# Kernel optimization log

Hardware: AMD Instinct MI355X
Metric: run time of the kernel (lower is better)

The kernel has to match this reference:

```python
import jax, jax.numpy as jnp
import numpy as np

B, STREAM, IN_CH = 128, 512, 4
EXTRA, GROUPS, DEPTH = 5, 2, 3
STEP, LENGTH = 16, 32
RNN, OUT = 256, 10
C = IN_CH + 1 + EXTRA              # augmented channels: original + time + 1x1-conv
SIG_C = C + C * C + C ** 3          # signature channels per group at depth 3
W = (STREAM - LENGTH) // STEP + 1   # number of sliding windows = GRU steps
F = GROUPS * SIG_C                  # GRU input features


def _outer(a, b):
    # flattened tensor (outer) product on last axis: (...,m),(...,n)->(...,m*n)
    return (a[..., :, None] * b[..., None, :]).reshape(a.shape[:-1] + (a.shape[-1] * b.shape[-1],))


def _chen_step(S, dx):
    # Chen's identity: S <- S (tensor) exp(dx). S is a tuple of flattened
    # signature levels (..., C^k), k=1..DEPTH; dx has shape (..., C).
    P = [jnp.ones(dx.shape[:-1] + (1,), dx.dtype)]  # dx^{(x)j}/j!, j=0..DEPTH
    for j in range(1, DEPTH + 1):
        P.append(_outer(P[-1], dx) / j)
    newS = []
    for k in range(1, DEPTH + 1):
        acc = P[k]  # S_0 (x) P_k
        for j in range(k):
            acc = acc + _outer(S[k - 1 - j], P[j])
        newS.append(acc)
    return tuple(newS)


def setup_inputs() -> dict:
    key = jax.random.key(0)
    ks = jax.random.split(key, 10)
    s_aug = 1.0 / np.sqrt(IN_CH)
    s_rnn = 1.0 / np.sqrt(RNN)
    return {
        "x": jax.random.normal(ks[0], (B, STREAM, IN_CH), jnp.float32),
        "W_aug": jax.random.uniform(ks[1], (GROUPS, EXTRA, IN_CH), jnp.float32, -s_aug, s_aug),
        "b_aug": jax.random.uniform(ks[2], (GROUPS, EXTRA), jnp.float32, -s_aug, s_aug),
        "W_ih": jax.random.uniform(ks[3], (3 * RNN, F), jnp.float32, -s_rnn, s_rnn),
        "W_hh": jax.random.uniform(ks[4], (3 * RNN, RNN), jnp.float32, -s_rnn, s_rnn),
        "b_ih": jax.random.uniform(ks[5], (3 * RNN,), jnp.float32, -s_rnn, s_rnn),
        "b_hh": jax.random.uniform(ks[6], (3 * RNN,), jnp.float32, -s_rnn, s_rnn),
        "W_out": jax.random.uniform(ks[7], (OUT, RNN), jnp.float32, -s_rnn, s_rnn),
        "b_out": jax.random.uniform(ks[8], (OUT,), jnp.float32, -s_rnn, s_rnn),
    }


def reference(x, W_aug, b_aug, W_ih, W_hh, b_ih, b_hh, W_out, b_out):
    # (a) linear augmentation per channel group: [original | time | conv1x1(x)]
    t = jnp.linspace(0.0, 1.0, STREAM, dtype=x.dtype)
    t = jnp.broadcast_to(t[None, :, None], (B, STREAM, 1))
    aug = jnp.einsum('bsi,gei->bgse', x, W_aug) + b_aug[None, :, None, :]  # (B,G,S,EXTRA)
    base = jnp.broadcast_to(jnp.concatenate([x, t], -1)[:, None],
                            (B, GROUPS, STREAM, IN_CH + 1))
    xa = jnp.concatenate([base, aug], -1)            # (B,G,S,C)
    xa = xa.reshape(B * GROUPS, STREAM, C)

    # (b) depth-3 signatures over sliding windows via Chen's identity
    dx = xa[:, 1:] - xa[:, :-1]                       # (BG, S-1, C)
    widx = jnp.arange(W)[:, None] * STEP + jnp.arange(LENGTH - 1)[None, :]
    dxw = dx[:, widx]                                 # (BG, W, L-1, C)
    dxw = jnp.moveaxis(dxw, 2, 0)                     # (L-1, BG, W, C)
    S0 = tuple(jnp.zeros((B * GROUPS, W, C ** k), x.dtype) for k in range(1, DEPTH + 1))
    S, _ = jax.lax.scan(lambda S, d: (_chen_step(S, d), None), S0, dxw)
    sig = jnp.concatenate(S, -1)                      # (BG, W, SIG_C)
    sig = sig.reshape(B, GROUPS, W, SIG_C)
    sig = jnp.moveaxis(sig, 2, 0).reshape(W, B, F)    # (W, B, G*SIG_C)

    # (c) GRU over window signatures (torch.nn.GRUCell math, gate order r,z,n)
    def gru(h, xt):
        gi = xt @ W_ih.T + b_ih
        gh = h @ W_hh.T + b_hh
        ir, iz, inn = jnp.split(gi, 3, -1)
        hr, hz, hn = jnp.split(gh, 3, -1)
        r = jax.nn.sigmoid(ir + hr)
        z = jax.nn.sigmoid(iz + hz)
        n = jnp.tanh(inn + r * hn)
        return (1 - z) * n + z * h, None

    h, _ = jax.lax.scan(gru, jnp.zeros((B, RNN), x.dtype), sig)
    return jax.nn.sigmoid(h @ W_out.T + b_out)        # (B, OUT)
```

## Files before the change

### kernel.cpp

```cpp
#include <hip/hip_runtime.h>
#include <hip/hip_bf16.h>
#include <stdint.h>


typedef _Float16 f16;
typedef f16  f16x2 __attribute__((ext_vector_type(2)));
typedef f16  f16x4 __attribute__((ext_vector_type(4)));
typedef f16  f16x8 __attribute__((ext_vector_type(8)));
typedef float f32x2 __attribute__((ext_vector_type(2)));
typedef float f32x4 __attribute__((ext_vector_type(4)));

#define ASYNC16(gp, lp) __builtin_amdgcn_global_load_lds( \
    (const __attribute__((address_space(1))) void*)(gp),  \
    (__attribute__((address_space(3))) void*)(lp), 16, 0, 0)

#define BAR_LDS() do { asm volatile("s_waitcnt lgkmcnt(0)" ::: "memory"); \
                       __builtin_amdgcn_s_barrier();                      \
                       asm volatile("" ::: "memory"); } while (0)

__device__ __forceinline__ float fexp2(float x) {
    float r; asm("v_exp_f32 %0, %1" : "=v"(r) : "v"(x)); return r;
}
__device__ __forceinline__ float frcp(float x) {
    float r; asm("v_rcp_f32 %0, %1" : "=v"(r) : "v"(x)); return r;
}

__global__ __launch_bounds__(256) void prep_kernel(const float* __restrict__ x,
                                                   const float* __restrict__ W_aug,
                                                   const float* __restrict__ Wih,
                                                   const float* __restrict__ Whh,
                                                   f16* __restrict__ sig16,
                                                   f16* __restrict__ wih16,
                                                   f16* __restrict__ whh16,
                                                   uint8_t* __restrict__ whh8) {
    __shared__ float dxs[4][31][10];
    __shared__ f16 srow[4][1112];
    const int tid = threadIdx.x;
    if (blockIdx.x < 840) {
        int c = blockIdx.x * 256 + tid;
        int r = c / 280, kc = (c - r * 280) * 8;
        const float* src = Wih + (size_t)r * 2220 + kc;
        f16x8 o;
        if (kc + 8 <= 2220) {
            float4 v0 = *(const float4*)(src);
            float4 v1 = *(const float4*)(src + 4);
            o[0]=(f16)v0.x; o[1]=(f16)v0.y; o[2]=(f16)v0.z; o[3]=(f16)v0.w;
            o[4]=(f16)v1.x; o[5]=(f16)v1.y; o[6]=(f16)v1.z; o[7]=(f16)v1.w;
        } else {
#pragma unroll
            for (int j = 0; j < 8; j++)
                o[j] = (f16)((kc + j < 2220) ? src[j] : 0.0f);
        }
        *(f16x8*)(wih16 + (size_t)r * 2240 + kc) = o;
        return;
    }
    if (blockIdx.x < 936) {
        int c2 = ((int)blockIdx.x - 840) * 256 + tid;
        int j8 = c2 * 8;
        float w[8];
        {
            float4 v0 = *(const float4*)(Whh + j8);
            float4 v1 = *(const float4*)(Whh + j8 + 4);
            w[0]=v0.x; w[1]=v0.y; w[2]=v0.z; w[3]=v0.w;
            w[4]=v1.x; w[5]=v1.y; w[6]=v1.z; w[7]=v1.w;
        }
        f16x8 o;
#pragma unroll
        for (int j = 0; j < 8; j++) o[j] = (f16)w[j];
        *(f16x8*)(whh16 + j8) = o;
        if (j8 < 131072) {
            uint32_t p01 = (uint32_t)__builtin_amdgcn_cvt_pk_fp8_f32(w[0]*16.f, w[1]*16.f, 0, false) & 0xffffu;
            uint32_t p23 = (uint32_t)__builtin_amdgcn_cvt_pk_fp8_f32(w[2]*16.f, w[3]*16.f, 0, false) & 0xffffu;
            uint32_t p45 = (uint32_t)__builtin_amdgcn_cvt_pk_fp8_f32(w[4]*16.f, w[5]*16.f, 0, false) & 0xffffu;
            uint32_t p67 = (uint32_t)__builtin_amdgcn_cvt_pk_fp8_f32(w[6]*16.f, w[7]*16.f, 0, false) & 0xffffu;
            uint2 st = make_uint2(p01 | (p23 << 16), p45 | (p67 << 16));
            *(uint2*)(whh8 + j8) = st;
        }
        return;
    }
    const int sub = tid >> 6, t64 = tid & 63;
    const int cid = ((int)blockIdx.x - 936) * 4 + sub;
    const int w = cid % 31;
    const int bg = cid / 31;
    const int b = bg >> 1, g = bg & 1;
    if (t64 < 31) {
        int s = w * 16 + t64;
        const float4 x0 = *(const float4*)(x + ((size_t)b * 512 + s) * 4);
        const float4 x1 = *(const float4*)(x + ((size_t)b * 512 + s + 1) * 4);
        float d0 = x1.x - x0.x, d1 = x1.y - x0.y, d2 = x1.z - x0.z, d3 = x1.w - x0.w;
        dxs[sub][t64][0] = d0; dxs[sub][t64][1] = d1;
        dxs[sub][t64][2] = d2; dxs[sub][t64][3] = d3;
        dxs[sub][t64][4] = 1.0f / 511.0f;
#pragma unroll
        for (int e = 0; e < 5; e++) {
            const float* wa = W_aug + (g * 5 + e) * 4;
            dxs[sub][t64][5 + e] = d0 * wa[0] + d1 * wa[1] + d2 * wa[2] + d3 * wa[3];
        }
    }
    __syncthreads();
    size_t base = ((size_t)(w * 128 + b)) * 2240 + (size_t)g * 1110;
    if (t64 < 50) {
        int p0 = 2 * t64, p1 = p0 + 1;
        int i0 = p0 / 10, j0 = p0 % 10, j1 = j0 + 1;
        const float* dz  = &dxs[sub][0][0];
        const float* pI  = dz + i0;
        const float* pJ0 = dz + j0;
        const float* pJ1 = dz + j1;
        float s3a[10], s3b[10];
#pragma unroll
        for (int k = 0; k < 10; k++) { s3a[k] = 0.f; s3b[k] = 0.f; }
        float s2a = 0.f, s2b = 0.f, s1 = 0.f;
        for (int l = 0; l < 31; l++) {
            const float* row = dz + l * 10;
            float di  = pI[l * 10];
            float dj0 = pJ0[l * 10];
            float dj1 = pJ1[l * 10];
            float t0 = s1 + di * (1.0f / 3.0f);
            float a0 = s2a + t0 * (0.5f * dj0);
            float a1 = s2b + t0 * (0.5f * dj1);
#pragma unroll
            for (int k = 0; k < 10; k++) {
                float dk = row[k];
                s3a[k] += a0 * dk;
                s3b[k] += a1 * dk;
            }
            float u = s1 + 0.5f * di;
            s2a += u * dj0;
            s2b += u * dj1;
            s1 += di;
        }
        *(f16x2*)&srow[sub][10 + p0] = (f16x2){(f16)s2a, (f16)s2b};
#pragma unroll
        for (int k = 0; k < 5; k++)
            *(f16x2*)&srow[sub][110 + p0 * 10 + 2 * k] =
                (f16x2){(f16)s3a[2 * k], (f16)s3a[2 * k + 1]};
#pragma unroll
        for (int k = 0; k < 5; k++)
            *(f16x2*)&srow[sub][110 + p1 * 10 + 2 * k] =
                (f16x2){(f16)s3b[2 * k], (f16)s3b[2 * k + 1]};
    } else if (t64 < 60) {
        int c = t64 - 50;
        const float* pc = &dxs[sub][0][0] + c;
        float s = 0.f;
        for (int l = 0; l < 31; l++) s += pc[l * 10];
        srow[sub][c] = (f16)s;
    }
    __syncthreads();
    for (int j = t64; j < 555; j += 64)
        *(f16x2*)(sig16 + base + 2 * j) = *(const f16x2*)&srow[sub][2 * j];
    if (g == 1 && t64 < 10)
        *(f16x2*)(sig16 + ((size_t)(w * 128 + b)) * 2240 + 2220 + 2 * t64) =
            (f16x2){(f16)0.0f, (f16)0.0f};
}

__global__ __launch_bounds__(256) void gemm_kernel(const f16* __restrict__ A,
                                                   const f16* __restrict__ Bw,
                                                   const float* __restrict__ bias,
                                                   const float* __restrict__ bhh,
                                                   f16* __restrict__ Cgi) {
    const int lin = blockIdx.x;
    const int nc = lin % 12;
    const int mb = lin / 12;
    const int t = mb >> 1, half = mb & 1;
    __shared__ __align__(16) f16 As[6][64 * 32];
    __shared__ __align__(16) f16 Bs[6][64 * 32];
    const int tid = threadIdx.x, lane = tid & 63, wid = tid >> 6;
    const int l16 = lane & 15, quad = lane >> 4;
    const int lrow = lane >> 2, lk = lane & 3;
    const int Nbase = nc * 64;
    const f16* gaA = A  + (size_t)(mb * 64 + wid * 16 + lrow) * 2240 + lk * 8;
    const f16* gbB = Bw + (size_t)(Nbase + wid * 16 + lrow) * 2240 + lk * 8;

#define GISSUE(KT, BUF) do { \
        int _k0 = (KT) * 32; \
        ASYNC16(gaA + _k0, &As[BUF][(wid * 16) * 32]); \
        ASYNC16(gbB + _k0, &Bs[BUF][(wid * 16) * 32]); } while (0)

#define GCOMPUTE(BUF) do { \
        f16x8 af, bf[4]; \
        af = *(const f16x8*)&As[BUF][(wid * 16 + l16) * 32 + quad * 8]; \
        _Pragma("unroll") \
        for (int nt = 0; nt < 4; nt++) \
            bf[nt] = *(const f16x8*)&Bs[BUF][(nt * 16 + l16) * 32 + quad * 8]; \
        _Pragma("unroll") \
        for (int nt = 0; nt < 4; nt++) \
            acc[nt] = __builtin_amdgcn_mfma_f32_16x16x32_f16(af, bf[nt], acc[nt], 0, 0, 0); } while (0)

    f32x4 acc[4];
#pragma unroll
    for (int nt = 0; nt < 4; nt++) acc[nt] = (f32x4){0.f, 0.f, 0.f, 0.f};

    GISSUE(0, 0); GISSUE(1, 1); GISSUE(2, 2); GISSUE(3, 3); GISSUE(4, 4);
    for (int kt = 0; kt < 65; kt++) {
        asm volatile("s_waitcnt vmcnt(8) lgkmcnt(0)\n\ts_barrier" ::: "memory");
        GISSUE(kt + 5, (kt + 5) % 6);
        GCOMPUTE(kt % 6);
    }
    asm volatile("s_waitcnt vmcnt(8) lgkmcnt(0)\n\ts_barrier" ::: "memory");
    GCOMPUTE(5);
    asm volatile("s_waitcnt vmcnt(6) lgkmcnt(0)\n\ts_barrier" ::: "memory");
    GCOMPUTE(0);
    asm volatile("s_waitcnt vmcnt(4) lgkmcnt(0)\n\ts_barrier" ::: "memory");
    GCOMPUTE(1);
    asm volatile("s_waitcnt vmcnt(2) lgkmcnt(0)\n\ts_barrier" ::: "memory");
    GCOMPUTE(2);
    asm volatile("s_waitcnt vmcnt(0) lgkmcnt(0)\n\ts_barrier" ::: "memory");
    GCOMPUTE(3);

    const float NEG_LOG2E = -1.4426950408889634f;
    const float TWO_LOG2E =  2.8853900817779268f;
    const int bbv = half * 4 + wid;
#pragma unroll
    for (int nt = 0; nt < 4; nt++) {
        int col = Nbase + nt * 16 + l16;
        float bvv = bias[col] + (col < 512 ? bhh[col] : 0.0f);
        float scl = (col < 512) ? NEG_LOG2E : TWO_LOG2E;
        int gs = col >> 8, hcc = col & 255;
        int gw = hcc >> 5, gtc = (hcc >> 4) & 1, gl = hcc & 15;
        int u = gs * 2 + gtc;
        int gtid = gw * 64 + quad * 16 + gl;
        size_t off = ((size_t)((t * 8 + bbv) * 6 + u)) * 2048 + (size_t)gtid * 4;
        f16x4 st;
#pragma unroll
        for (int rr = 0; rr < 4; rr++) st[rr] = (f16)((acc[nt][rr] + bvv) * scl);
        *(f16x4*)(Cgi + off) = st;
    }
#undef GISSUE
#undef GCOMPUTE
}

#define ACLOB \
  "a0","a1","a2","a3","a4","a5","a6","a7","a8","a9","a10","a11","a12","a13","a14","a15", \
  "a16","a17","a18","a19","a20","a21","a22","a23","a24","a25","a26","a27","a28","a29","a30","a31", \
  "a32","a33","a34","a35","a36","a37","a38","a39","a40","a41","a42","a43","a44","a45","a46","a47", \
  "a48","a49","a50","a51","a52","a53","a54","a55","a56","a57","a58","a59","a60","a61","a62","a63", \
  "a64","a65","a66","a67","a68","a69","a70","a71","a72","a73","a74","a75","a76","a77","a78","a79", \
  "a80","a81","a82","a83","a84","a85","a86","a87","a88","a89","a90","a91","a92","a93","a94","a95", \
  "a96","a97","a98","a99","a100","a101","a102","a103","a104","a105","a106","a107","a108","a109","a110","a111", \
  "a112","a113","a114","a115","a116","a117","a118","a119","a120","a121","a122","a123","a124","a125","a126","a127"

#define LF8(A0,A1, U, KT) do { \
  f32x2 _t = *(const f32x2*)(whh8 + (size_t)(((U) >> 1) * 256 + wid * 32 + ((U) & 1) * 16 + l16) * 256 + (KT) * 32 + quad * 8); \
  asm volatile("v_accvgpr_write_b32 a" #A0 ", %0\n\t" \
               "v_accvgpr_write_b32 a" #A1 ", %1" \
               :: "v"(_t[0]), "v"(_t[1]) : "a" #A0, "a" #A1); } while (0)

#define LFN(A0,A1,A2,A3, TC, KT) do { \
  f32x4 _t = *(const f32x4*)(whh16 + (size_t)(512 + wid * 32 + (TC) * 16 + l16) * 256 + (KT) * 32 + quad * 8); \
  asm volatile("v_accvgpr_write_b32 a" #A0 ", %0\n\t" \
               "v_accvgpr_write_b32 a" #A1 ", %1\n\t" \
               "v_accvgpr_write_b32 a" #A2 ", %2\n\t" \
               "v_accvgpr_write_b32 a" #A3 ", %3" \
               :: "v"(_t[0]), "v"(_t[1]), "v"(_t[2]), "v"(_t[3]) \
               : "a" #A0, "a" #A1, "a" #A2, "a" #A3); } while (0)

#define FP8GZ(P, F0,F1,F2,F3) \
  "v_mfma_f32_16x16x32_fp8_fp8 %[aR0], " P ", a[" F0 "], %[zq]\n\t" \
  "v_mfma_f32_16x16x32_fp8_fp8 %[aR1], " P ", a[" F1 "], %[zq]\n\t" \
  "v_mfma_f32_16x16x32_fp8_fp8 %[aZ0], " P ", a[" F2 "], %[zq]\n\t" \
  "v_mfma_f32_16x16x32_fp8_fp8 %[aZ1], " P ", a[" F3 "], %[zq]\n\t"

#define FP8G(P, F0,F1,F2,F3) \
  "v_mfma_f32_16x16x32_fp8_fp8 %[aR0], " P ", a[" F0 "], %[aR0]\n\t" \
  "v_mfma_f32_16x16x32_fp8_fp8 %[aR1], " P ", a[" F1 "], %[aR1]\n\t" \
  "v_mfma_f32_16x16x32_fp8_fp8 %[aZ0], " P ", a[" F2 "], %[aZ0]\n\t" \
  "v_mfma_f32_16x16x32_fp8_fp8 %[aZ1], " P ", a[" F3 "], %[aZ1]\n\t"

#define F16GZ(Q, G0,G1) \
  "v_mfma_f32_16x16x32_f16 %[aN0], " Q ", a[" G0 "], %[zq]\n\t" \
  "v_mfma_f32_16x16x32_f16 %[aN1], " Q ", a[" G1 "], %[zq]\n\t"

#define F16G(Q, G0,G1) \
  "v_mfma_f32_16x16x32_f16 %[aN0], " Q ", a[" G0 "], %[aN0]\n\t" \
  "v_mfma_f32_16x16x32_f16 %[aN1], " Q ", a[" G1 "], %[aN1]\n\t"

__global__ __launch_bounds__(512, 2) void gru_kernel(const f16* __restrict__ gi,
                                                     const f16* __restrict__ whh16,
                                                     const uint8_t* __restrict__ whh8,
                                                     const float* __restrict__ b_hh,
                                                     const float* __restrict__ W_out,
                                                     const float* __restrict__ b_out,
                                                     float* __restrict__ out) {
    __shared__ __align__(16) f16 hbufF[2][16 * 280];
    __shared__ __align__(16) uint8_t hbuf8[2][16 * 272];
    const int tid = threadIdx.x, lane = tid & 63, wid = tid >> 6;
    const int quad = lane >> 4, l16 = lane & 15;
    const int bb = blockIdx.x;

    for (int i = tid; i < 16 * 280; i += 512) hbufF[1][i] = (f16)0.0f;
    for (int i = tid; i < 16 * 272; i += 512) hbuf8[1][i] = 0;

    LF8(0,1, 0,0);   LF8(2,3, 0,1);   LF8(4,5, 0,2);   LF8(6,7, 0,3);
    LF8(8,9, 0,4);   LF8(10,11, 0,5); LF8(12,13, 0,6); LF8(14,15, 0,7);
    LF8(16,17, 1,0); LF8(18,19, 1,1); LF8(20,21, 1,2); LF8(22,23, 1,3);
    LF8(24,25, 1,4); LF8(26,27, 1,5); LF8(28,29, 1,6); LF8(30,31, 1,7);
    LF8(32,33, 2,0); LF8(34,35, 2,1); LF8(36,37, 2,2); LF8(38,39, 2,3);
    LF8(40,41, 2,4); LF8(42,43, 2,5); LF8(44,45, 2,6); LF8(46,47, 2,7);
    LF8(48,49, 3,0); LF8(50,51, 3,1); LF8(52,53, 3,2); LF8(54,55, 3,3);
    LF8(56,57, 3,4); LF8(58,59, 3,5); LF8(60,61, 3,6); LF8(62,63, 3,7);
    LFN(64,65,66,67,   0,0); LFN(68,69,70,71,   0,1); LFN(72,73,74,75,   0,2); LFN(76,77,78,79,   0,3);
    LFN(80,81,82,83,   0,4); LFN(84,85,86,87,   0,5); LFN(88,89,90,91,   0,6); LFN(92,93,94,95,   0,7);
    LFN(96,97,98,99,   1,0); LFN(100,101,102,103, 1,1); LFN(104,105,106,107, 1,2); LFN(108,109,110,111, 1,3);
    LFN(112,113,114,115, 1,4); LFN(116,117,118,119, 1,5); LFN(120,121,122,123, 1,6); LFN(124,125,126,127, 1,7);

    const float C2 = 2.8853900817779268f;
    float bhn[2];
#pragma unroll
    for (int tc = 0; tc < 2; tc++) bhn[tc] = C2 * b_hh[512 + wid * 32 + tc * 16 + l16];
    float hm[2][4];
#pragma unroll
    for (int tc = 0; tc < 2; tc++)
#pragma unroll
        for (int rr = 0; rr < 4; rr++) hm[tc][rr] = 0.f;

    uint32_t aF0 = (uint32_t)(uintptr_t)(__attribute__((address_space(3))) const void*)
                       (&hbufF[0][l16 * 280 + quad * 8]);
    uint32_t aF1 = (uint32_t)(uintptr_t)(__attribute__((address_space(3))) const void*)
                       (&hbufF[1][l16 * 280 + quad * 8]);
    uint32_t a80 = (uint32_t)(uintptr_t)(__attribute__((address_space(3))) const void*)
                       (&hbuf8[0][l16 * 272 + quad * 8]);
    uint32_t a81 = (uint32_t)(uintptr_t)(__attribute__((address_space(3))) const void*)
                       (&hbuf8[1][l16 * 272 + quad * 8]);

    const size_t lanebase = (size_t)bb * 12288 + (size_t)tid * 4;
    f16x4 gcur[6];
#pragma unroll
    for (int u = 0; u < 6; u++)
        gcur[u] = *(const f16x4*)(gi + lanebase + u * 2048);

    const f32x4 zq = (f32x4){0.f, 0.f, 0.f, 0.f};

    BAR_LDS();

    for (int t = 0; t < 31; t++) {
        const uint32_t a8 = (t & 1) ? a80 : a81;
        const uint32_t aF = (t & 1) ? aF0 : aF1;
        f32x4 aR0, aR1, aZ0, aZ1, aN0, aN1;
        f32x2 p0, p1, p2;
        f32x4 q0, q1, q2;
        asm volatile(
            "s_setprio 1\n\t"
            "ds_read_b64  %[p0], %[a8] offset:0\n\t"
            "ds_read_b128 %[q0], %[aF] offset:0\n\t"
            "ds_read_b64  %[p1], %[a8] offset:32\n\t"
            "ds_read_b128 %[q1], %[aF] offset:64\n\t"
            "ds_read_b64  %[p2], %[a8] offset:64\n\t"
            "ds_read_b128 %[q2], %[aF] offset:128\n\t"
            "s_waitcnt lgkmcnt(5)\n\t"
            FP8GZ("%[p0]", "0:1","16:17","32:33","48:49")
            "ds_read_b64  %[p0], %[a8] offset:96\n\t"
            "s_waitcnt lgkmcnt(5)\n\t"
            F16GZ("%[q0]", "64:67","96:99")
            "ds_read_b128 %[q0], %[aF] offset:192\n\t"
            "s_waitcnt lgkmcnt(5)\n\t"
            FP8G("%[p1]", "2:3","18:19","34:35","50:51")
            "ds_read_b64  %[p1], %[a8] offset:128\n\t"
            "s_waitcnt lgkmcnt(5)\n\t"
            F16G("%[q1]", "68:71","100:103")
            "ds_read_b128 %[q1], %[aF] offset:256\n\t"
            "s_waitcnt lgkmcnt(5)\n\t"
            FP8G("%[p2]", "4:5","20:21","36:37","52:53")
            "ds_read_b64  %[p2], %[a8] offset:160\n\t"
            "s_waitcnt lgkmcnt(5)\n\t"
            F16G("%[q2]", "72:75","104:107")
            "ds_read_b128 %[q2], %[aF] offset:320\n\t"
            "s_waitcnt lgkmcnt(5)\n\t"
            FP8G("%[p0]", "6:7","22:23","38:39","54:55")
            "ds_read_b64  %[p0], %[a8] offset:192\n\t"
            "s_waitcnt lgkmcnt(5)\n\t"
            F16G("%[q0]", "76:79","108:111")
            "ds_read_b128 %[q0], %[aF] offset:384\n\t"
            "s_waitcnt lgkmcnt(5)\n\t"
            FP8G("%[p1]", "8:9","24:25","40:41","56:57")
            "ds_read_b64  %[p1], %[a8] offset:224\n\t"
            "s_waitcnt lgkmcnt(5)\n\t"
            F16G("%[q1]", "80:83","112:115")
            "ds_read_b128 %[q1], %[aF] offset:448\n\t"
            "s_waitcnt lgkmcnt(5)\n\t"
            FP8G("%[p2]", "10:11","26:27","42:43","58:59")
            "s_waitcnt lgkmcnt(4)\n\t"
            F16G("%[q2]", "84:87","116:119")
            "s_waitcnt lgkmcnt(3)\n\t"
            FP8G("%[p0]", "12:13","28:29","44:45","60:61")
            "s_waitcnt lgkmcnt(2)\n\t"
            F16G("%[q0]", "88:91","120:123")
            "s_waitcnt lgkmcnt(1)\n\t"
            FP8G("%[p1]", "14:15","30:31","46:47","62:63")
            "s_waitcnt lgkmcnt(0)\n\t"
            F16G("%[q1]", "92:95","124:127")
            "s_setprio 0\n\t"
            "s_nop 7\n\ts_nop 7"
            : [aR0]"=&v"(aR0), [aR1]"=&v"(aR1), [aZ0]"=&v"(aZ0), [aZ1]"=&v"(aZ1),
              [aN0]"=&v"(aN0), [aN1]"=&v"(aN1),
              [p0]"=&v"(p0), [p1]"=&v"(p1), [p2]"=&v"(p2),
              [q0]"=&v"(q0), [q1]"=&v"(q1), [q2]"=&v"(q2)
            : [a8]"v"(a8), [aF]"v"(aF), [zq]"v"(zq)
            : ACLOB);

        f16* hdF = hbufF[t & 1];
        uint8_t* hd8 = hbuf8[t & 1];
        const float C1N16 = -0.09016844005556021f;
#pragma unroll
        for (int tc = 0; tc < 2; tc++) {
            const int hcx = wid * 32 + tc * 16 + l16;
            const f32x4 vR = tc ? aR1 : aR0;
            const f32x4 vZ = tc ? aZ1 : aZ0;
            const f32x4 vN = tc ? aN1 : aN0;
#pragma unroll
            for (int rr = 0; rr < 4; rr++) {
                float rg = frcp(1.f + fexp2(fmaf(C1N16, vR[rr], (float)gcur[tc][rr])));
                float zg = frcp(1.f + fexp2(fmaf(C1N16, vZ[rr], (float)gcur[2 + tc][rr])));
                float t2 = fmaf(rg, fmaf(C2, vN[rr], bhn[tc]), (float)gcur[4 + tc][rr]);
                float e2 = fexp2(t2);
                float ng = fmaf(-2.f, frcp(e2 + 1.f), 1.f);
                float h  = fmaf(zg, hm[tc][rr] - ng, ng);
                hm[tc][rr] = h;
                hdF[(quad * 4 + rr) * 280 + hcx] = (f16)h;
                int pk = __builtin_amdgcn_cvt_pk_fp8_f32(h, h, 0, false);
                hd8[(quad * 4 + rr) * 272 + hcx] = (uint8_t)pk;
            }
        }
        {
            int tn = (t < 30) ? t + 1 : 30;
            const f16* gsrc = gi + (size_t)tn * 98304 + lanebase;
#pragma unroll
            for (int u = 0; u < 6; u++)
                gcur[u] = *(const f16x4*)(gsrc + u * 2048);
        }
        BAR_LDS();
    }
    if (tid < 160) {
        int r = tid / 10, oc = tid - r * 10;
        const f16* hfin = hbufF[0];
        float s = b_out[oc];
        for (int k = 0; k < 256; k++) s += (float)hfin[r * 280 + k] * W_out[oc * 256 + k];
        out[(bb * 16 + r) * 10 + oc] = frcp(1.f + __expf(-s));
    }
}

extern "C" void kernel_launch(void* const* d_in, const int* in_sizes, int n_in,
                              void* d_out, int out_size, void* d_ws, size_t ws_size,
                              hipStream_t stream) {
    const float* x     = (const float*)d_in[0];
    const float* W_aug = (const float*)d_in[1];
    const float* W_ih  = (const float*)d_in[3];
    const float* W_hh  = (const float*)d_in[4];
    const float* b_ih  = (const float*)d_in[5];
    const float* b_hh  = (const float*)d_in[6];
    const float* W_out = (const float*)d_in[7];
    const float* b_out = (const float*)d_in[8];
    float* out = (float*)d_out;

    char* ws = (char*)d_ws;
    const size_t SIG_BYTES  = (size_t)3968 * 2240 * 2;
    const size_t WIH_BYTES  = (size_t)768 * 2240 * 2;
    const size_t WHH_BYTES  = (size_t)768 * 256 * 2;
    const size_t WHH8_BYTES = (size_t)512 * 256;
    const size_t GI_BYTES   = (size_t)31 * 8 * 6 * 512 * 4 * 2;
    if (ws_size < SIG_BYTES + WIH_BYTES + WHH_BYTES + WHH8_BYTES + GI_BYTES) return;
    f16* sig16    = (f16*)ws;
    f16* wih16    = (f16*)(ws + SIG_BYTES);
    f16* whh16    = (f16*)(ws + SIG_BYTES + WIH_BYTES);
    uint8_t* whh8 = (uint8_t*)(ws + SIG_BYTES + WIH_BYTES + WHH_BYTES);
    f16* giw      = (f16*)(ws + SIG_BYTES + WIH_BYTES + WHH_BYTES + WHH8_BYTES);

    hipLaunchKernelGGL(prep_kernel, dim3(2920), dim3(256), 0, stream,
                       x, W_aug, W_ih, W_hh, sig16, wih16, whh16, whh8);
    hipLaunchKernelGGL(gemm_kernel, dim3(744), dim3(256), 0, stream,
                       sig16, wih16, b_ih, b_hh, giw);
    hipLaunchKernelGGL(gru_kernel, dim3(8), dim3(512), 0, stream,
                       giw, whh16, whh8, b_hh, W_out, b_out, out);
}
```

Baseline: 196.4 us.

## Split GRU recurrence across 16 waves with half the hidden columns each

```diff
diff --git a/kernel.cpp b/kernel.cpp
--- a/kernel.cpp
+++ b/kernel.cpp
@@ -229,24 +229,20 @@
 #undef GCOMPUTE
 }
 
-#define ACLOB \
+#define ACLOB64 \
   "a0","a1","a2","a3","a4","a5","a6","a7","a8","a9","a10","a11","a12","a13","a14","a15", \
   "a16","a17","a18","a19","a20","a21","a22","a23","a24","a25","a26","a27","a28","a29","a30","a31", \
   "a32","a33","a34","a35","a36","a37","a38","a39","a40","a41","a42","a43","a44","a45","a46","a47", \
-  "a48","a49","a50","a51","a52","a53","a54","a55","a56","a57","a58","a59","a60","a61","a62","a63", \
-  "a64","a65","a66","a67","a68","a69","a70","a71","a72","a73","a74","a75","a76","a77","a78","a79", \
-  "a80","a81","a82","a83","a84","a85","a86","a87","a88","a89","a90","a91","a92","a93","a94","a95", \
-  "a96","a97","a98","a99","a100","a101","a102","a103","a104","a105","a106","a107","a108","a109","a110","a111", \
-  "a112","a113","a114","a115","a116","a117","a118","a119","a120","a121","a122","a123","a124","a125","a126","a127"
-
-#define LF8(A0,A1, U, KT) do { \
-  f32x2 _t = *(const f32x2*)(whh8 + (size_t)(((U) >> 1) * 256 + wid * 32 + ((U) & 1) * 16 + l16) * 256 + (KT) * 32 + quad * 8); \
+  "a48","a49","a50","a51","a52","a53","a54","a55","a56","a57","a58","a59","a60","a61","a62","a63"
+
+#define LF8(A0,A1, G, KT) do { \
+  f32x2 _t = *(const f32x2*)(whh8 + (size_t)((G) * 256 + wid * 16 + l16) * 256 + (KT) * 32 + quad * 8); \
   asm volatile("v_accvgpr_write_b32 a" #A0 ", %0\n\t" \
                "v_accvgpr_write_b32 a" #A1 ", %1" \
                :: "v"(_t[0]), "v"(_t[1]) : "a" #A0, "a" #A1); } while (0)
 
-#define LFN(A0,A1,A2,A3, TC, KT) do { \
-  f32x4 _t = *(const f32x4*)(whh16 + (size_t)(512 + wid * 32 + (TC) * 16 + l16) * 256 + (KT) * 32 + quad * 8); \
+#define LFN(A0,A1,A2,A3, KT) do { \
+  f32x4 _t = *(const f32x4*)(whh16 + (size_t)(512 + wid * 16 + l16) * 256 + (KT) * 32 + quad * 8); \
   asm volatile("v_accvgpr_write_b32 a" #A0 ", %0\n\t" \
                "v_accvgpr_write_b32 a" #A1 ", %1\n\t" \
                "v_accvgpr_write_b32 a" #A2 ", %2\n\t" \
@@ -254,64 +250,49 @@
                :: "v"(_t[0]), "v"(_t[1]), "v"(_t[2]), "v"(_t[3]) \
                : "a" #A0, "a" #A1, "a" #A2, "a" #A3); } while (0)
 
-#define FP8GZ(P, F0,F1,F2,F3) \
-  "v_mfma_f32_16x16x32_fp8_fp8 %[aR0], " P ", a[" F0 "], %[zq]\n\t" \
-  "v_mfma_f32_16x16x32_fp8_fp8 %[aR1], " P ", a[" F1 "], %[zq]\n\t" \
-  "v_mfma_f32_16x16x32_fp8_fp8 %[aZ0], " P ", a[" F2 "], %[zq]\n\t" \
-  "v_mfma_f32_16x16x32_fp8_fp8 %[aZ1], " P ", a[" F3 "], %[zq]\n\t"
-
-#define FP8G(P, F0,F1,F2,F3) \
-  "v_mfma_f32_16x16x32_fp8_fp8 %[aR0], " P ", a[" F0 "], %[aR0]\n\t" \
-  "v_mfma_f32_16x16x32_fp8_fp8 %[aR1], " P ", a[" F1 "], %[aR1]\n\t" \
-  "v_mfma_f32_16x16x32_fp8_fp8 %[aZ0], " P ", a[" F2 "], %[aZ0]\n\t" \
-  "v_mfma_f32_16x16x32_fp8_fp8 %[aZ1], " P ", a[" F3 "], %[aZ1]\n\t"
-
-#define F16GZ(Q, G0,G1) \
-  "v_mfma_f32_16x16x32_f16 %[aN0], " Q ", a[" G0 "], %[zq]\n\t" \
-  "v_mfma_f32_16x16x32_f16 %[aN1], " Q ", a[" G1 "], %[zq]\n\t"
-
-#define F16G(Q, G0,G1) \
-  "v_mfma_f32_16x16x32_f16 %[aN0], " Q ", a[" G0 "], %[aN0]\n\t" \
-  "v_mfma_f32_16x16x32_f16 %[aN1], " Q ", a[" G1 "], %[aN1]\n\t"
-
-__global__ __launch_bounds__(512, 2) void gru_kernel(const f16* __restrict__ gi,
-                                                     const f16* __restrict__ whh16,
-                                                     const uint8_t* __restrict__ whh8,
-                                                     const float* __restrict__ b_hh,
-                                                     const float* __restrict__ W_out,
-                                                     const float* __restrict__ b_out,
-                                                     float* __restrict__ out) {
+#define RZGZ(P, F0,F1) \
+  "v_mfma_f32_16x16x32_fp8_fp8 %[aR], " P ", a[" F0 "], %[zq]\n\t" \
+  "v_mfma_f32_16x16x32_fp8_fp8 %[aZ], " P ", a[" F1 "], %[zq]\n\t"
+
+#define RZG(P, F0,F1) \
+  "v_mfma_f32_16x16x32_fp8_fp8 %[aR], " P ", a[" F0 "], %[aR]\n\t" \
+  "v_mfma_f32_16x16x32_fp8_fp8 %[aZ], " P ", a[" F1 "], %[aZ]\n\t"
+
+#define NGZ(Q, G0) \
+  "v_mfma_f32_16x16x32_f16 %[aN], " Q ", a[" G0 "], %[zq]\n\t"
+
+#define NG(Q, G0) \
+  "v_mfma_f32_16x16x32_f16 %[aN], " Q ", a[" G0 "], %[aN]\n\t"
+
+__global__ __launch_bounds__(1024, 4) void gru_kernel(const f16* __restrict__ gi,
+                                                      const f16* __restrict__ whh16,
+                                                      const uint8_t* __restrict__ whh8,
+                                                      const float* __restrict__ b_hh,
+                                                      const float* __restrict__ W_out,
+                                                      const float* __restrict__ b_out,
+                                                      float* __restrict__ out) {
     __shared__ __align__(16) f16 hbufF[2][16 * 280];
     __shared__ __align__(16) uint8_t hbuf8[2][16 * 272];
     const int tid = threadIdx.x, lane = tid & 63, wid = tid >> 6;
     const int quad = lane >> 4, l16 = lane & 15;
     const int bb = blockIdx.x;
 
-    for (int i = tid; i < 16 * 280; i += 512) hbufF[1][i] = (f16)0.0f;
-    for (int i = tid; i < 16 * 272; i += 512) hbuf8[1][i] = 0;
-
-    LF8(0,1, 0,0);   LF8(2,3, 0,1);   LF8(4,5, 0,2);   LF8(6,7, 0,3);
-    LF8(8,9, 0,4);   LF8(10,11, 0,5); LF8(12,13, 0,6); LF8(14,15, 0,7);
+    for (int i = tid; i < 16 * 280; i += 1024) hbufF[1][i] = (f16)0.0f;
+    for (int i = tid; i < 16 * 272; i += 1024) hbuf8[1][i] = 0;
+
+    LF8(0,1,   0,0); LF8(2,3,   0,1); LF8(4,5,   0,2); LF8(6,7,   0,3);
+    LF8(8,9,   0,4); LF8(10,11, 0,5); LF8(12,13, 0,6); LF8(14,15, 0,7);
     LF8(16,17, 1,0); LF8(18,19, 1,1); LF8(20,21, 1,2); LF8(22,23, 1,3);
     LF8(24,25, 1,4); LF8(26,27, 1,5); LF8(28,29, 1,6); LF8(30,31, 1,7);
-    LF8(32,33, 2,0); LF8(34,35, 2,1); LF8(36,37, 2,2); LF8(38,39, 2,3);
-    LF8(40,41, 2,4); LF8(42,43, 2,5); LF8(44,45, 2,6); LF8(46,47, 2,7);
-    LF8(48,49, 3,0); LF8(50,51, 3,1); LF8(52,53, 3,2); LF8(54,55, 3,3);
-    LF8(56,57, 3,4); LF8(58,59, 3,5); LF8(60,61, 3,6); LF8(62,63, 3,7);
-    LFN(64,65,66,67,   0,0); LFN(68,69,70,71,   0,1); LFN(72,73,74,75,   0,2); LFN(76,77,78,79,   0,3);
-    LFN(80,81,82,83,   0,4); LFN(84,85,86,87,   0,5); LFN(88,89,90,91,   0,6); LFN(92,93,94,95,   0,7);
-    LFN(96,97,98,99,   1,0); LFN(100,101,102,103, 1,1); LFN(104,105,106,107, 1,2); LFN(108,109,110,111, 1,3);
-    LFN(112,113,114,115, 1,4); LFN(116,117,118,119, 1,5); LFN(120,121,122,123, 1,6); LFN(124,125,126,127, 1,7);
+    LFN(32,33,34,35, 0); LFN(36,37,38,39, 1); LFN(40,41,42,43, 2); LFN(44,45,46,47, 3);
+    LFN(48,49,50,51, 4); LFN(52,53,54,55, 5); LFN(56,57,58,59, 6); LFN(60,61,62,63, 7);
 
     const float C2 = 2.8853900817779268f;
-    float bhn[2];
-#pragma unroll
-    for (int tc = 0; tc < 2; tc++) bhn[tc] = C2 * b_hh[512 + wid * 32 + tc * 16 + l16];
-    float hm[2][4];
-#pragma unroll
-    for (int tc = 0; tc < 2; tc++)
-#pragma unroll
-        for (int rr = 0; rr < 4; rr++) hm[tc][rr] = 0.f;
+    const int hcx = wid * 16 + l16;
+    const float bhn = C2 * b_hh[512 + hcx];
+    float hm[4];
+#pragma unroll
+    for (int rr = 0; rr < 4; rr++) hm[rr] = 0.f;
 
     uint32_t aF0 = (uint32_t)(uintptr_t)(__attribute__((address_space(3))) const void*)
                        (&hbufF[0][l16 * 280 + quad * 8]);
@@ -322,11 +303,12 @@
     uint32_t a81 = (uint32_t)(uintptr_t)(__attribute__((address_space(3))) const void*)
                        (&hbuf8[1][l16 * 272 + quad * 8]);
 
-    const size_t lanebase = (size_t)bb * 12288 + (size_t)tid * 4;
-    f16x4 gcur[6];
-#pragma unroll
-    for (int u = 0; u < 6; u++)
-        gcur[u] = *(const f16x4*)(gi + lanebase + u * 2048);
+    const size_t lanebase = (size_t)bb * 12288 + (size_t)(wid & 1) * 2048
+                          + (size_t)((wid >> 1) * 64 + quad * 16 + l16) * 4;
+    f16x4 gcur[3];
+#pragma unroll
+    for (int gs = 0; gs < 3; gs++)
+        gcur[gs] = *(const f16x4*)(gi + lanebase + (size_t)gs * 4096);
 
     const f32x4 zq = (f32x4){0.f, 0.f, 0.f, 0.f};
 
@@ -335,7 +317,7 @@
     for (int t = 0; t < 31; t++) {
         const uint32_t a8 = (t & 1) ? a80 : a81;
         const uint32_t aF = (t & 1) ? aF0 : aF1;
-        f32x4 aR0, aR1, aZ0, aZ1, aN0, aN1;
+        f32x4 aR, aZ, aN;
         f32x2 p0, p1, p2;
         f32x4 q0, q1, q2;
         asm volatile(
@@ -347,85 +329,77 @@
             "ds_read_b64  %[p2], %[a8] offset:64\n\t"
             "ds_read_b128 %[q2], %[aF] offset:128\n\t"
             "s_waitcnt lgkmcnt(5)\n\t"
-            FP8GZ("%[p0]", "0:1","16:17","32:33","48:49")
+            RZGZ("%[p0]", "0:1", "16:17")
             "ds_read_b64  %[p0], %[a8] offset:96\n\t"
             "s_waitcnt lgkmcnt(5)\n\t"
-            F16GZ("%[q0]", "64:67","96:99")
+            NGZ("%[q0]", "32:35")
             "ds_read_b128 %[q0], %[aF] offset:192\n\t"
             "s_waitcnt lgkmcnt(5)\n\t"
-            FP8G("%[p1]", "2:3","18:19","34:35","50:51")
+            RZG("%[p1]", "2:3", "18:19")
             "ds_read_b64  %[p1], %[a8] offset:128\n\t"
             "s_waitcnt lgkmcnt(5)\n\t"
-            F16G("%[q1]", "68:71","100:103")
+            NG("%[q1]", "36:39")
             "ds_read_b128 %[q1], %[aF] offset:256\n\t"
             "s_waitcnt lgkmcnt(5)\n\t"
-            FP8G("%[p2]", "4:5","20:21","36:37","52:53")
+            RZG("%[p2]", "4:5", "20:21")
             "ds_read_b64  %[p2], %[a8] offset:160\n\t"
             "s_waitcnt lgkmcnt(5)\n\t"
-            F16G("%[q2]", "72:75","104:107")
+            NG("%[q2]", "40:43")
             "ds_read_b128 %[q2], %[aF] offset:320\n\t"
             "s_waitcnt lgkmcnt(5)\n\t"
-            FP8G("%[p0]", "6:7","22:23","38:39","54:55")
+            RZG("%[p0]", "6:7", "22:23")
             "ds_read_b64  %[p0], %[a8] offset:192\n\t"
             "s_waitcnt lgkmcnt(5)\n\t"
-            F16G("%[q0]", "76:79","108:111")
+            NG("%[q0]", "44:47")
             "ds_read_b128 %[q0], %[aF] offset:384\n\t"
             "s_waitcnt lgkmcnt(5)\n\t"
-            FP8G("%[p1]", "8:9","24:25","40:41","56:57")
+            RZG("%[p1]", "8:9", "24:25")
             "ds_read_b64  %[p1], %[a8] offset:224\n\t"
             "s_waitcnt lgkmcnt(5)\n\t"
-            F16G("%[q1]", "80:83","112:115")
+            NG("%[q1]", "48:51")
             "ds_read_b128 %[q1], %[aF] offset:448\n\t"
             "s_waitcnt lgkmcnt(5)\n\t"
-            FP8G("%[p2]", "10:11","26:27","42:43","58:59")
+            RZG("%[p2]", "10:11", "26:27")
             "s_waitcnt lgkmcnt(4)\n\t"
-            F16G("%[q2]", "84:87","116:119")
+            NG("%[q2]", "52:55")
             "s_waitcnt lgkmcnt(3)\n\t"
-            FP8G("%[p0]", "12:13","28:29","44:45","60:61")
+            RZG("%[p0]", "12:13", "28:29")
             "s_waitcnt lgkmcnt(2)\n\t"
-            F16G("%[q0]", "88:91","120:123")
+            NG("%[q0]", "56:59")
             "s_waitcnt lgkmcnt(1)\n\t"
-            FP8G("%[p1]", "14:15","30:31","46:47","62:63")
+            RZG("%[p1]", "14:15", "30:31")
             "s_waitcnt lgkmcnt(0)\n\t"
-            F16G("%[q1]", "92:95","124:127")
+            NG("%[q1]", "60:63")
             "s_setprio 0\n\t"
             "s_nop 7\n\ts_nop 7"
-            : [aR0]"=&v"(aR0), [aR1]"=&v"(aR1), [aZ0]"=&v"(aZ0), [aZ1]"=&v"(aZ1),
-              [aN0]"=&v"(aN0), [aN1]"=&v"(aN1),
+            : [aR]"=&v"(aR), [aZ]"=&v"(aZ), [aN]"=&v"(aN),
               [p0]"=&v"(p0), [p1]"=&v"(p1), [p2]"=&v"(p2),
               [q0]"=&v"(q0), [q1]"=&v"(q1), [q2]"=&v"(q2)
             : [a8]"v"(a8), [aF]"v"(aF), [zq]"v"(zq)
-            : ACLOB);
+            : ACLOB64);
 
         f16* hdF = hbufF[t & 1];
         uint8_t* hd8 = hbuf8[t & 1];
         const float C1N16 = -0.09016844005556021f;
 #pragma unroll
-        for (int tc = 0; tc < 2; tc++) {
-            const int hcx = wid * 32 + tc * 16 + l16;
-            const f32x4 vR = tc ? aR1 : aR0;
-            const f32x4 vZ = tc ? aZ1 : aZ0;
-            const f32x4 vN = tc ? aN1 : aN0;
-#pragma unroll
-            for (int rr = 0; rr < 4; rr++) {
-                float rg = frcp(1.f + fexp2(fmaf(C1N16, vR[rr], (float)gcur[tc][rr])));
-                float zg = frcp(1.f + fexp2(fmaf(C1N16, vZ[rr], (float)gcur[2 + tc][rr])));
-                float t2 = fmaf(rg, fmaf(C2, vN[rr], bhn[tc]), (float)gcur[4 + tc][rr]);
-                float e2 = fexp2(t2);
-                float ng = fmaf(-2.f, frcp(e2 + 1.f), 1.f);
-                float h  = fmaf(zg, hm[tc][rr] - ng, ng);
-                hm[tc][rr] = h;
-                hdF[(quad * 4 + rr) * 280 + hcx] = (f16)h;
-                int pk = __builtin_amdgcn_cvt_pk_fp8_f32(h, h, 0, false);
-                hd8[(quad * 4 + rr) * 272 + hcx] = (uint8_t)pk;
-            }
+        for (int rr = 0; rr < 4; rr++) {
+            float rg = frcp(1.f + fexp2(fmaf(C1N16, aR[rr], (float)gcur[0][rr])));
+            float zg = frcp(1.f + fexp2(fmaf(C1N16, aZ[rr], (float)gcur[1][rr])));
+            float t2 = fmaf(rg, fmaf(C2, aN[rr], bhn), (float)gcur[2][rr]);
+            float e2 = fexp2(t2);
+            float ng = fmaf(-2.f, frcp(e2 + 1.f), 1.f);
+            float h  = fmaf(zg, hm[rr] - ng, ng);
+            hm[rr] = h;
+            hdF[(quad * 4 + rr) * 280 + hcx] = (f16)h;
+            int pk = __builtin_amdgcn_cvt_pk_fp8_f32(h, h, 0, false);
+            hd8[(quad * 4 + rr) * 272 + hcx] = (uint8_t)pk;
         }
         {
             int tn = (t < 30) ? t + 1 : 30;
             const f16* gsrc = gi + (size_t)tn * 98304 + lanebase;
 #pragma unroll
-            for (int u = 0; u < 6; u++)
-                gcur[u] = *(const f16x4*)(gsrc + u * 2048);
+            for (int gs = 0; gs < 3; gs++)
+                gcur[gs] = *(const f16x4*)(gsrc + (size_t)gs * 4096);
         }
         BAR_LDS();
     }
@@ -468,6 +442,6 @@
                        x, W_aug, W_ih, W_hh, sig16, wih16, whh16, whh8);
     hipLaunchKernelGGL(gemm_kernel, dim3(744), dim3(256), 0, stream,
                        sig16, wih16, b_ih, b_hh, giw);
-    hipLaunchKernelGGL(gru_kernel, dim3(8), dim3(512), 0, stream,
+    hipLaunchKernelGGL(gru_kernel, dim3(8), dim3(1024), 0, stream,
                        giw, whh16, whh8, b_hh, W_out, b_out, out);
 }
```

Result: no change. 199.2 us (+1.5%).

## Split GEMM K dimension across two wave groups with LDS reduction

Applied to the files above, without the earlier changes.

```diff
diff --git a/kernel.cpp b/kernel.cpp
--- a/kernel.cpp
+++ b/kernel.cpp
@@ -153,7 +153,7 @@
             (f16x2){(f16)0.0f, (f16)0.0f};
 }
 
-__global__ __launch_bounds__(256) void gemm_kernel(const f16* __restrict__ A,
+__global__ __launch_bounds__(512) void gemm_kernel(const f16* __restrict__ A,
                                                    const f16* __restrict__ Bw,
                                                    const float* __restrict__ bias,
                                                    const float* __restrict__ bhh,
@@ -162,26 +162,28 @@
     const int nc = lin % 12;
     const int mb = lin / 12;
     const int t = mb >> 1, half = mb & 1;
-    __shared__ __align__(16) f16 As[6][64 * 32];
-    __shared__ __align__(16) f16 Bs[6][64 * 32];
+    __shared__ __align__(16) f16 As[2][3][64 * 32];
+    __shared__ __align__(16) f16 Bs[2][3][64 * 32];
+    __shared__ __align__(16) float sc[4][16 * 64];
     const int tid = threadIdx.x, lane = tid & 63, wid = tid >> 6;
+    const int kh = wid >> 2, w4 = wid & 3;
     const int l16 = lane & 15, quad = lane >> 4;
     const int lrow = lane >> 2, lk = lane & 3;
     const int Nbase = nc * 64;
-    const f16* gaA = A  + (size_t)(mb * 64 + wid * 16 + lrow) * 2240 + lk * 8;
-    const f16* gbB = Bw + (size_t)(Nbase + wid * 16 + lrow) * 2240 + lk * 8;
+    const f16* gaA = A  + (size_t)(mb * 64 + w4 * 16 + lrow) * 2240 + kh * 1120 + lk * 8;
+    const f16* gbB = Bw + (size_t)(Nbase + w4 * 16 + lrow) * 2240 + kh * 1120 + lk * 8;
 
 #define GISSUE(KT, BUF) do { \
         int _k0 = (KT) * 32; \
-        ASYNC16(gaA + _k0, &As[BUF][(wid * 16) * 32]); \
-        ASYNC16(gbB + _k0, &Bs[BUF][(wid * 16) * 32]); } while (0)
+        ASYNC16(gaA + _k0, &As[kh][BUF][(w4 * 16) * 32]); \
+        ASYNC16(gbB + _k0, &Bs[kh][BUF][(w4 * 16) * 32]); } while (0)
 
 #define GCOMPUTE(BUF) do { \
         f16x8 af, bf[4]; \
-        af = *(const f16x8*)&As[BUF][(wid * 16 + l16) * 32 + quad * 8]; \
+        af = *(const f16x8*)&As[kh][BUF][(w4 * 16 + l16) * 32 + quad * 8]; \
         _Pragma("unroll") \
         for (int nt = 0; nt < 4; nt++) \
-            bf[nt] = *(const f16x8*)&Bs[BUF][(nt * 16 + l16) * 32 + quad * 8]; \
+            bf[nt] = *(const f16x8*)&Bs[kh][BUF][(nt * 16 + l16) * 32 + quad * 8]; \
         _Pragma("unroll") \
         for (int nt = 0; nt < 4; nt++) \
             acc[nt] = __builtin_amdgcn_mfma_f32_16x16x32_f16(af, bf[nt], acc[nt], 0, 0, 0); } while (0)
@@ -190,40 +192,47 @@
 #pragma unroll
     for (int nt = 0; nt < 4; nt++) acc[nt] = (f32x4){0.f, 0.f, 0.f, 0.f};
 
-    GISSUE(0, 0); GISSUE(1, 1); GISSUE(2, 2); GISSUE(3, 3); GISSUE(4, 4);
-    for (int kt = 0; kt < 65; kt++) {
-        asm volatile("s_waitcnt vmcnt(8) lgkmcnt(0)\n\ts_barrier" ::: "memory");
-        GISSUE(kt + 5, (kt + 5) % 6);
-        GCOMPUTE(kt % 6);
-    }
-    asm volatile("s_waitcnt vmcnt(8) lgkmcnt(0)\n\ts_barrier" ::: "memory");
-    GCOMPUTE(5);
-    asm volatile("s_waitcnt vmcnt(6) lgkmcnt(0)\n\ts_barrier" ::: "memory");
+    GISSUE(0, 0); GISSUE(1, 1);
+    for (int kt = 0; kt < 33; kt++) {
+        asm volatile("s_waitcnt vmcnt(2) lgkmcnt(0)\n\ts_barrier" ::: "memory");
+        GISSUE(kt + 2, (kt + 2) % 3);
+        GCOMPUTE(kt % 3);
+    }
+    asm volatile("s_waitcnt vmcnt(2) lgkmcnt(0)\n\ts_barrier" ::: "memory");
     GCOMPUTE(0);
-    asm volatile("s_waitcnt vmcnt(4) lgkmcnt(0)\n\ts_barrier" ::: "memory");
+    asm volatile("s_waitcnt vmcnt(0) lgkmcnt(0)\n\ts_barrier" ::: "memory");
     GCOMPUTE(1);
-    asm volatile("s_waitcnt vmcnt(2) lgkmcnt(0)\n\ts_barrier" ::: "memory");
-    GCOMPUTE(2);
-    asm volatile("s_waitcnt vmcnt(0) lgkmcnt(0)\n\ts_barrier" ::: "memory");
-    GCOMPUTE(3);
-
-    const float NEG_LOG2E = -1.4426950408889634f;
-    const float TWO_LOG2E =  2.8853900817779268f;
-    const int bbv = half * 4 + wid;
-#pragma unroll
-    for (int nt = 0; nt < 4; nt++) {
-        int col = Nbase + nt * 16 + l16;
-        float bvv = bias[col] + (col < 512 ? bhh[col] : 0.0f);
-        float scl = (col < 512) ? NEG_LOG2E : TWO_LOG2E;
-        int gs = col >> 8, hcc = col & 255;
-        int gw = hcc >> 5, gtc = (hcc >> 4) & 1, gl = hcc & 15;
-        int u = gs * 2 + gtc;
-        int gtid = gw * 64 + quad * 16 + gl;
-        size_t off = ((size_t)((t * 8 + bbv) * 6 + u)) * 2048 + (size_t)gtid * 4;
-        f16x4 st;
-#pragma unroll
-        for (int rr = 0; rr < 4; rr++) st[rr] = (f16)((acc[nt][rr] + bvv) * scl);
-        *(f16x4*)(Cgi + off) = st;
+
+    if (kh == 1) {
+#pragma unroll
+        for (int nt = 0; nt < 4; nt++)
+#pragma unroll
+            for (int rr = 0; rr < 4; rr++)
+                sc[w4][(quad * 4 + rr) * 64 + nt * 16 + l16] = acc[nt][rr];
+    }
+    __syncthreads();
+    if (kh == 0) {
+        const float NEG_LOG2E = -1.4426950408889634f;
+        const float TWO_LOG2E =  2.8853900817779268f;
+        const int bbv = half * 4 + w4;
+#pragma unroll
+        for (int nt = 0; nt < 4; nt++) {
+            int col = Nbase + nt * 16 + l16;
+            float bvv = bias[col] + (col < 512 ? bhh[col] : 0.0f);
+            float scl = (col < 512) ? NEG_LOG2E : TWO_LOG2E;
+            int gs = col >> 8, hcc = col & 255;
+            int gw = hcc >> 5, gtc = (hcc >> 4) & 1, gl = hcc & 15;
+            int u = gs * 2 + gtc;
+            int gtid = gw * 64 + quad * 16 + gl;
+            size_t off = ((size_t)((t * 8 + bbv) * 6 + u)) * 2048 + (size_t)gtid * 4;
+            f16x4 st;
+#pragma unroll
+            for (int rr = 0; rr < 4; rr++) {
+                float v = acc[nt][rr] + sc[w4][(quad * 4 + rr) * 64 + nt * 16 + l16];
+                st[rr] = (f16)((v + bvv) * scl);
+            }
+            *(f16x4*)(Cgi + off) = st;
+        }
     }
 #undef GISSUE
 #undef GCOMPUTE
@@ -466,7 +475,7 @@
 
     hipLaunchKernelGGL(prep_kernel, dim3(2920), dim3(256), 0, stream,
                        x, W_aug, W_ih, W_hh, sig16, wih16, whh16, whh8);
-    hipLaunchKernelGGL(gemm_kernel, dim3(744), dim3(256), 0, stream,
+    hipLaunchKernelGGL(gemm_kernel, dim3(744), dim3(512), 0, stream,
                        sig16, wih16, b_ih, b_hh, giw);
     hipLaunchKernelGGL(gru_kernel, dim3(8), dim3(512), 0, stream,
                        giw, whh16, whh8, b_hh, W_out, b_out, out);
```

Measured after the change: 195.4 us. No clear change (-0.5%).
